# Kernel optimization log

Measured on AMD Instinct MI355X. Metric: run time of the kernel, lower is better.

The kernel has to match this reference:

```python
import jax, jax.numpy as jnp
import numpy as np

D_MODEL = 1024
N_HEADS = 16
HEAD_DIM = D_MODEL // N_HEADS
WINDOW = 128
N_PERSIST = 4
KSIZE = 3


def _make_mask(L):
    """[T,T] additive mask, T = N_PERSIST + L. Persistent rows: causal among
    persistent tokens. Sequence rows: all persistent cols + sliding causal window."""
    T = N_PERSIST + L
    r = jnp.arange(T)[:, None]
    c = jnp.arange(T)[None, :]
    seq_allowed = (c < N_PERSIST) | ((c >= jnp.maximum(N_PERSIST, r - WINDOW + 1)) & (c <= r))
    allowed = jnp.where(r < N_PERSIST, c <= r, seq_allowed)
    return jnp.where(allowed, 0.0, -jnp.inf).astype(jnp.float32)


def _causal_dw_conv(y, w, b):
    # y: [B,T,D] -> depthwise causal conv1d + SiLU -> [B,T,D]
    y = y.transpose(0, 2, 1)  # [B,D,T]
    y = jax.lax.conv_general_dilated(
        y, w, window_strides=(1,), padding=[(KSIZE - 1, 0)],
        feature_group_count=D_MODEL, dimension_numbers=('NCH', 'OIH', 'NCH'))
    y = jax.nn.silu(y + b[None, :, None])
    return y.transpose(0, 2, 1)


def _l2norm(y, eps=1e-12):
    n = jnp.linalg.norm(y, axis=-1, keepdims=True)
    return y / jnp.maximum(n, eps)


def setup_inputs() -> dict:
    key = jax.random.key(0)
    ks = jax.random.split(key, 12)
    s = 1.0 / np.sqrt(D_MODEL)
    return {
        'x': jax.random.normal(ks[0], (1, 2048, D_MODEL), jnp.float32),
        'persistent_memory': jax.random.normal(ks[1], (1, N_PERSIST, D_MODEL), jnp.float32) * 0.02,
        'Wq': jax.random.normal(ks[2], (D_MODEL, D_MODEL), jnp.float32) * s,
        'Wk': jax.random.normal(ks[3], (D_MODEL, D_MODEL), jnp.float32) * s,
        'Wv': jax.random.normal(ks[4], (D_MODEL, D_MODEL), jnp.float32) * s,
        'Wo': jax.random.normal(ks[5], (D_MODEL, D_MODEL), jnp.float32) * s,
        'q_conv_w': jax.random.normal(ks[6], (D_MODEL, 1, KSIZE), jnp.float32) * 0.3,
        'q_conv_b': jax.random.normal(ks[7], (D_MODEL,), jnp.float32) * 0.02,
        'k_conv_w': jax.random.normal(ks[8], (D_MODEL, 1, KSIZE), jnp.float32) * 0.3,
        'k_conv_b': jax.random.normal(ks[9], (D_MODEL,), jnp.float32) * 0.02,
        'v_conv_w': jax.random.normal(ks[10], (D_MODEL, 1, KSIZE), jnp.float32) * 0.3,
        'v_conv_b': jax.random.normal(ks[11], (D_MODEL,), jnp.float32) * 0.02,
    }


def reference(x, persistent_memory, Wq, Wk, Wv, Wo,
              q_conv_w, q_conv_b, k_conv_w, k_conv_b, v_conv_w, v_conv_b):
    B, L, D = x.shape
    T = L + N_PERSIST
    scale = HEAD_DIM ** -0.5
    xp = jnp.concatenate([jnp.broadcast_to(persistent_memory, (B, N_PERSIST, D)), x], axis=1)
    Q = xp @ Wq.T
    K = xp @ Wk.T
    V = xp @ Wv.T
    Q = _causal_dw_conv(Q, q_conv_w, q_conv_b)
    K = _causal_dw_conv(K, k_conv_w, k_conv_b)
    V = _causal_dw_conv(V, v_conv_w, v_conv_b)
    Q = _l2norm(Q)
    K = _l2norm(K)
    # [B,H,T,hd]
    Q = Q.reshape(B, T, N_HEADS, HEAD_DIM).transpose(0, 2, 1, 3)
    K = K.reshape(B, T, N_HEADS, HEAD_DIM).transpose(0, 2, 1, 3)
    V = V.reshape(B, T, N_HEADS, HEAD_DIM).transpose(0, 2, 1, 3)
    scores = jnp.einsum('bhqd,bhkd->bhqk', Q, K) * scale + _make_mask(L)[None, None]
    attn = jax.nn.softmax(scores, axis=-1)
    out = jnp.einsum('bhqk,bhkd->bhqd', attn, V)
    out = out.transpose(0, 2, 1, 3).reshape(B, T, D) @ Wo.T
    return out[:, N_PERSIST:, :]
```

## Files before the change

kernel.cpp:

```cpp
#include <hip/hip_runtime.h>
#include <math.h>

typedef unsigned short u16;
typedef unsigned int   u32;
typedef unsigned long long u64;
typedef __attribute__((ext_vector_type(8))) short bf16x8;
typedef __attribute__((ext_vector_type(4))) float f32x4;
typedef __attribute__((ext_vector_type(4))) int i32x4;

#define TTOT  2052
#define NPERS 4
#define LSEQ  2048
#define WIN   128
#define NHEAD 16
#define HDIM  64
#define DM    1024
#define MPAD  2176

__device__ __forceinline__ float bf2f(u16 u) {
    union { unsigned int i; float f; } v; v.i = ((unsigned int)u) << 16; return v.f;
}
__device__ __forceinline__ u16 f2bf(float f) {
    union { float f; unsigned int i; } v; v.f = f;
    unsigned int r = (v.i + 0x7fffu + ((v.i >> 16) & 1u)) >> 16;
    return (u16)r;
}
__device__ __forceinline__ u32 pk2(float lo, float hi) {
    return (u32)f2bf(lo) | ((u32)f2bf(hi) << 16);
}

__device__ __forceinline__ void glds16(const u16* g, u16* l) {
    __builtin_amdgcn_global_load_lds(
        (__attribute__((address_space(1))) void*)(g),
        (__attribute__((address_space(3))) void*)(l),
        16, 0, 0);
}

#define XP_UNITS (TTOT * DM / 4)
#define W_UNITS  (DM * DM / 4)
#define CVT_BLOCKS ((XP_UNITS + 4 * W_UNITS) / 256)

__global__ __launch_bounds__(256) void cvt(const float* __restrict__ x, const float* __restrict__ pm,
    const float* __restrict__ Wq, const float* __restrict__ Wk, const float* __restrict__ Wv,
    const float* __restrict__ Wo,
    u16* __restrict__ xp, u16* __restrict__ Wcat, u16* __restrict__ Woh)
{
    const int id = blockIdx.x * 256 + threadIdx.x;
    const float* s; u16* d;
    if (id < XP_UNITS) {
        const size_t e = (size_t)id * 4;
        const int row = (int)(e >> 10), c = (int)(e & 1023);
        s = (row < NPERS) ? (pm + (size_t)row * DM + c) : (x + (size_t)(row - NPERS) * DM + c);
        d = xp + e;
    } else {
        const int w   = id - XP_UNITS;
        const int sel = w >> 18;
        const size_t e = (size_t)(w & (W_UNITS - 1)) * 4;
        if (sel == 0)      { s = Wq + e; d = Wcat + e; }
        else if (sel == 1) { s = Wk + e; d = Wcat + (size_t)DM * DM + e; }
        else if (sel == 2) { s = Wv + e; d = Wcat + 2 * (size_t)DM * DM + e; }
        else               { s = Wo + e; d = Woh + e; }
    }
    f32x4 v = *(const f32x4*)s;
    *(u64*)d = (u64)pk2(v[0], v[1]) | ((u64)pk2(v[2], v[3]) << 32);
}

template<int TM, int TN, bool OF32>
__device__ __forceinline__ void gemm_lds(const u16* __restrict__ Ablk, const u16* __restrict__ Bblk,
                                         void* __restrict__ Cbase, int mlim)
{
    __shared__ __align__(16) u16 As[TM * 64];
    __shared__ __align__(16) u16 Bs[TN * 64];
    const int tid  = threadIdx.x;
    const int lane = tid & 63;
    const int l15  = lane & 15, quad = lane >> 4;
    constexpr int RM = TM / 32, RN = TN / 32;
    const int wm = (tid >> 7) * (TM / 2);
    const int wn = ((tid >> 6) & 1) * (TN / 2);

    f32x4 acc[RM][RN];
    #pragma unroll
    for (int i = 0; i < RM; i++)
        #pragma unroll
        for (int j = 0; j < RN; j++) acc[i][j] = (f32x4){0.f, 0.f, 0.f, 0.f};

    constexpr int LA = TM / 32;
    constexpr int LB = TN / 32;

    for (int kk = 0; kk < DM; kk += 64) {
        #pragma unroll
        for (int i = 0; i < LA; i++) {
            const int e = i * 256 + tid;
            const int row = e >> 3, sc = (e & 7) ^ (row & 7);
            glds16(Ablk + (size_t)row * DM + kk + sc * 8, As + (size_t)e * 8);
        }
        #pragma unroll
        for (int i = 0; i < LB; i++) {
            const int e = i * 256 + tid;
            const int row = e >> 3, sc = (e & 7) ^ (row & 7);
            glds16(Bblk + (size_t)row * DM + kk + sc * 8, Bs + (size_t)e * 8);
        }
        __syncthreads();
        #pragma unroll
        for (int kc = 0; kc < 2; kc++) {
            bf16x8 af[RM], bfr[RN];
            #pragma unroll
            for (int i = 0; i < RM; i++)
                af[i]  = *(const bf16x8*)&As[(wm + i * 16 + l15) * 64 + (((kc * 4 + quad) ^ (l15 & 7)) * 8)];
            #pragma unroll
            for (int j = 0; j < RN; j++)
                bfr[j] = *(const bf16x8*)&Bs[(wn + j * 16 + l15) * 64 + (((kc * 4 + quad) ^ (l15 & 7)) * 8)];
            #pragma unroll
            for (int i = 0; i < RM; i++)
                #pragma unroll
                for (int j = 0; j < RN; j++)
                    acc[i][j] = __builtin_amdgcn_mfma_f32_16x16x32_bf16(af[i], bfr[j], acc[i][j], 0, 0, 0);
        }
        __syncthreads();
    }

    #pragma unroll
    for (int i = 0; i < RM; i++) {
        const int m0 = wm + i * 16 + quad * 4;
        #pragma unroll
        for (int j = 0; j < RN; j++) {
            const int n = wn + j * 16 + l15;
            #pragma unroll
            for (int r = 0; r < 4; r++) {
                const int m = m0 + r;
                if (m < mlim) {
                    if (OF32) ((float*)Cbase)[(size_t)m * DM + n] = acc[i][j][r];
                    else      ((u16*)Cbase)[(size_t)m * DM + n]   = f2bf(acc[i][j][r]);
                }
            }
        }
    }
}

__global__ __launch_bounds__(256) void gemm_qkv(const u16* __restrict__ xp, const u16* __restrict__ Wcat,
    u16* __restrict__ Qr, u16* __restrict__ Kr, u16* __restrict__ Vr)
{
    const int Mb = blockIdx.x * 128;
    const int nb = blockIdx.y;
    u16* C = (nb < 8) ? Qr : (nb < 16) ? Kr : Vr;
    const int Ncol = (nb & 7) * 128;
    gemm_lds<128, 128, false>(xp + (size_t)Mb * DM,
                              Wcat + (size_t)nb * 128 * DM,
                              (void*)(C + (size_t)Mb * DM + Ncol),
                              TTOT - Mb);
}

__global__ __launch_bounds__(256) void gemm_out(const u16* __restrict__ AO, const u16* __restrict__ Woh,
                                                float* __restrict__ Cout)
{
    const int Mb = blockIdx.x * 64, Nb = blockIdx.y * 128;
    gemm_lds<64, 128, true>(AO + (size_t)Mb * DM, Woh + (size_t)Nb * DM,
                            (void*)(Cout + (size_t)Mb * DM + Nb), 64);
}

__global__ __launch_bounds__(256) void conv_silu_norm(
    const u16* __restrict__ Qr, const u16* __restrict__ Kr, const u16* __restrict__ Vr,
    const float* __restrict__ qw, const float* __restrict__ qb,
    const float* __restrict__ kw, const float* __restrict__ kb,
    const float* __restrict__ vw, const float* __restrict__ vb,
    u16* __restrict__ Qc, u16* __restrict__ Kc, u16* __restrict__ Vc)
{
    const int t0 = blockIdx.x * 2;
    const int z  = blockIdx.y;
    const u16* raw; const float *w, *b; u16* out;
    if (z == 0)      { raw = Qr; w = qw; b = qb; out = Qc; }
    else if (z == 1) { raw = Kr; w = kw; b = kb; out = Kc; }
    else             { raw = Vr; w = vw; b = vb; out = Vc; }

    const int tid = threadIdx.x;
    const int d0  = tid * 4;

    const u16* r0 = raw + (size_t)t0 * DM + d0;
    const u64 cm2 = (t0 >= 2) ? *(const u64*)(r0 - 2 * DM) : 0ULL;
    const u64 cm1 = (t0 >= 1) ? *(const u64*)(r0 - DM)     : 0ULL;
    const u64 c0  = *(const u64*)r0;
    const u64 c1  = *(const u64*)(r0 + DM);
    const f32x4 bias = *(const f32x4*)(b + d0);
    const f32x4 w0v  = *(const f32x4*)(w + 3 * d0);
    const f32x4 w1v  = *(const f32x4*)(w + 3 * d0 + 4);
    const f32x4 w2v  = *(const f32x4*)(w + 3 * d0 + 8);
    const float warr[12] = {w0v[0], w0v[1], w0v[2], w0v[3],
                            w1v[0], w1v[1], w1v[2], w1v[3],
                            w2v[0], w2v[1], w2v[2], w2v[3]};

    float va[4], vb2[4];
    float ss0 = 0.f, ss1 = 0.f;
    #pragma unroll
    for (int c = 0; c < 4; c++) {
        const float xm2 = bf2f((u16)(cm2 >> (16 * c)));
        const float xm1 = bf2f((u16)(cm1 >> (16 * c)));
        const float x0  = bf2f((u16)(c0  >> (16 * c)));
        const float x1  = bf2f((u16)(c1  >> (16 * c)));
        const float w0 = warr[3*c], w1 = warr[3*c + 1], w2 = warr[3*c + 2];
        float a0 = bias[c] + w2 * x0 + w1 * xm1 + w0 * xm2;
        float a1 = bias[c] + w2 * x1 + w1 * x0  + w0 * xm1;
        const float y0 = a0 / (1.f + __expf(-a0));
        const float y1 = a1 / (1.f + __expf(-a1));
        va[c] = y0; vb2[c] = y1;
        ss0 += y0 * y0; ss1 += y1 * y1;
    }
    float inv0 = 1.f, inv1 = 1.f;
    if (z < 2) {
        #pragma unroll
        for (int off = 32; off > 0; off >>= 1) {
            ss0 += __shfl_down(ss0, off, 64);
            ss1 += __shfl_down(ss1, off, 64);
        }
        __shared__ float red[8];
        const int wv = tid >> 6, ln = tid & 63;
        if (ln == 0) { red[wv] = ss0; red[wv + 4] = ss1; }
        __syncthreads();
        inv0 = 1.f / fmaxf(sqrtf(red[0] + red[1] + red[2] + red[3]), 1e-12f);
        inv1 = 1.f / fmaxf(sqrtf(red[4] + red[5] + red[6] + red[7]), 1e-12f);
    }
    u64 o0 = 0, o1 = 0;
    #pragma unroll
    for (int c = 0; c < 4; c++) {
        o0 |= (u64)f2bf(va[c]  * inv0) << (16 * c);
        o1 |= (u64)f2bf(vb2[c] * inv1) << (16 * c);
    }
    *(u64*)(out + (size_t)t0 * DM + d0)      = o0;
    *(u64*)(out + (size_t)(t0 + 1) * DM + d0) = o1;
}

#define QT     64
#define KTILES 13
#define KROWS  208
#define KPAD   224
#define KSTR   72
#define VSTR   232

__global__ __launch_bounds__(256) void attn(const u16* __restrict__ Q, const u16* __restrict__ K,
                                            const u16* __restrict__ V, u16* __restrict__ AO)
{
    const int h  = blockIdx.y;
    const int qb = blockIdx.x * QT;
    const int kstart = max(NPERS, qb + NPERS - (WIN - 1));
    const int nk = NPERS + (qb + NPERS + QT - 1) - kstart + 1;

    __shared__ __align__(16) u16 KP[KROWS * KSTR];
    __shared__ __align__(16) u16 Vt[64 * VSTR];
    u16* Ks = KP;
    u16* Ps = KP;

    const int tid = threadIdx.x;

    for (int c = tid; c < KROWS * 8; c += 256) {
        const int i = c >> 3, off = (c & 7) * 8;
        if (i < nk) {
            const int g = (i < NPERS) ? i : (kstart + i - NPERS);
            *(i32x4*)&Ks[i * KSTR + off] = *(const i32x4*)&K[(size_t)g * DM + h * HDIM + off];
        }
    }
    {
        const int d = tid & 63, w4 = tid >> 6;
        for (int i2 = w4 * 2; i2 < KPAD; i2 += 8) {
            u16 a = 0, b = 0;
            if (i2 < nk)     { const int g = (i2     < NPERS) ? i2     : (kstart + i2     - NPERS); a = V[(size_t)g * DM + h * HDIM + d]; }
            if (i2 + 1 < nk) { const int g = (i2 + 1 < NPERS) ? i2 + 1 : (kstart + i2 + 1 - NPERS); b = V[(size_t)g * DM + h * HDIM + d]; }
            *(u32*)&Vt[d * VSTR + i2] = (u32)a | ((u32)b << 16);
        }
    }
    __syncthreads();

    const int wv = tid >> 6, lane = tid & 63, l15 = lane & 15, quad = lane >> 4;
    const int qloc0 = wv * 16;

    const int tqrow = qb + qloc0 + l15 + NPERS;
    const bf16x8 qa0 = *(const bf16x8*)&Q[(size_t)tqrow * DM + h * HDIM + quad * 8];
    const bf16x8 qa1 = *(const bf16x8*)&Q[(size_t)tqrow * DM + h * HDIM + 32 + quad * 8];

    f32x4 st[KTILES];
    #pragma unroll
    for (int t = 0; t < KTILES; t++) {
        const bf16x8 kb0 = *(const bf16x8*)&Ks[(t * 16 + l15) * KSTR + quad * 8];
        const bf16x8 kb1 = *(const bf16x8*)&Ks[(t * 16 + l15) * KSTR + 32 + quad * 8];
        f32x4 z = (f32x4){0.f, 0.f, 0.f, 0.f};
        z = __builtin_amdgcn_mfma_f32_16x16x32_bf16(qa0, kb0, z, 0, 0, 0);
        z = __builtin_amdgcn_mfma_f32_16x16x32_bf16(qa1, kb1, z, 0, 0, 0);
        st[t] = z;
    }

    const float scale = 0.125f;
    float mrow[4] = {-INFINITY, -INFINITY, -INFINITY, -INFINITY};
    #pragma unroll
    for (int t = 0; t < KTILES; t++) {
        const int i  = t * 16 + l15;
        const int kg = kstart + i - NPERS;
        #pragma unroll
        for (int r = 0; r < 4; r++) {
            const int tqr = qb + qloc0 + quad * 4 + r + NPERS;
            const bool ok = (i < NPERS) || ((i < nk) && (kg >= tqr - (WIN - 1)) && (kg <= tqr));
            const float s = ok ? st[t][r] * scale : -INFINITY;
            st[t][r] = s;
            mrow[r] = fmaxf(mrow[r], s);
        }
    }
    #pragma unroll
    for (int off = 1; off < 16; off <<= 1)
        #pragma unroll
        for (int r = 0; r < 4; r++) mrow[r] = fmaxf(mrow[r], __shfl_xor(mrow[r], off, 64));

    float ssum[4] = {0.f, 0.f, 0.f, 0.f};
    #pragma unroll
    for (int t = 0; t < KTILES; t++)
        #pragma unroll
        for (int r = 0; r < 4; r++) {
            const float p = __expf(st[t][r] - mrow[r]);
            st[t][r] = p;
            ssum[r] += p;
        }
    #pragma unroll
    for (int off = 1; off < 16; off <<= 1)
        #pragma unroll
        for (int r = 0; r < 4; r++) ssum[r] += __shfl_xor(ssum[r], off, 64);
    float inv[4];
    #pragma unroll
    for (int r = 0; r < 4; r++) inv[r] = 1.f / ssum[r];

    __syncthreads();

    #pragma unroll
    for (int t = 0; t < KTILES; t++)
        #pragma unroll
        for (int r = 0; r < 4; r++)
            Ps[(qloc0 + quad * 4 + r) * VSTR + t * 16 + l15] = f2bf(st[t][r] * inv[r]);
    *(u64*)&Ps[(qloc0 + l15) * VSTR + KROWS + quad * 4] = 0ULL;
    __syncthreads();

    f32x4 oacc[4];
    #pragma unroll
    for (int dt = 0; dt < 4; dt++) oacc[dt] = (f32x4){0.f, 0.f, 0.f, 0.f};
    for (int ks = 0; ks < KPAD / 32; ks++) {
        const bf16x8 pa = *(const bf16x8*)&Ps[(qloc0 + l15) * VSTR + ks * 32 + quad * 8];
        #pragma unroll
        for (int dt = 0; dt < 4; dt++) {
            const bf16x8 vb = *(const bf16x8*)&Vt[(dt * 16 + l15) * VSTR + ks * 32 + quad * 8];
            oacc[dt] = __builtin_amdgcn_mfma_f32_16x16x32_bf16(pa, vb, oacc[dt], 0, 0, 0);
        }
    }

    #pragma unroll
    for (int dt = 0; dt < 4; dt++)
        #pragma unroll
        for (int r = 0; r < 4; r++)
            AO[(size_t)(qb + qloc0 + quad * 4 + r) * DM + h * HDIM + dt * 16 + l15] = f2bf(oacc[dt][r]);
}

extern "C" void kernel_launch(void* const* d_in, const int* in_sizes, int n_in,
                              void* d_out, int out_size, void* d_ws, size_t ws_size,
                              hipStream_t stream)
{
    const float* x  = (const float*)d_in[0];
    const float* pm = (const float*)d_in[1];
    const float* Wq = (const float*)d_in[2];
    const float* Wk = (const float*)d_in[3];
    const float* Wv = (const float*)d_in[4];
    const float* Wo = (const float*)d_in[5];
    const float* qw = (const float*)d_in[6];
    const float* qb = (const float*)d_in[7];
    const float* kw = (const float*)d_in[8];
    const float* kb = (const float*)d_in[9];
    const float* vw = (const float*)d_in[10];
    const float* vb = (const float*)d_in[11];
    float* out = (float*)d_out;

    u16* ws16 = (u16*)d_ws;
    const size_t SZ_W  = (size_t)DM * DM;
    const size_t SZ_R  = (size_t)TTOT * DM;
    const size_t SZ_XP = (size_t)MPAD * DM;
    u16* Woh  = ws16;
    u16* Qr   = Woh + SZ_W;        u16* AO = Qr;
    u16* Kr   = Qr + SZ_R;
    u16* Vr   = Kr + SZ_R;
    u16* Vc   = Vr + SZ_R;
    u16* xp   = Vc + SZ_R;         u16* Qc = xp;
    u16* Wcat = xp + SZ_XP;        u16* Kc = Wcat;

    hipLaunchKernelGGL(cvt, dim3(CVT_BLOCKS), dim3(256), 0, stream,
                       x, pm, Wq, Wk, Wv, Wo, xp, Wcat, Woh);
    hipLaunchKernelGGL(gemm_qkv, dim3(17, 24), dim3(256), 0, stream,
                       xp, Wcat, Qr, Kr, Vr);
    hipLaunchKernelGGL(conv_silu_norm, dim3(TTOT / 2, 3), dim3(256), 0, stream,
                       Qr, Kr, Vr, qw, qb, kw, kb, vw, vb, Qc, Kc, Vc);
    hipLaunchKernelGGL(attn, dim3(LSEQ / QT, NHEAD), dim3(256), 0, stream,
                       Qc, Kc, Vc, AO);
    hipLaunchKernelGGL(gemm_out, dim3(32, 8), dim3(256), 0, stream,
                       AO, Woh, out);
}
```

Before: 159.2 us.

## Prefetch V into registers, async swizzled K load, drop softmax max pass

The attention kernel now issues the V gathers into registers up front and writes them to the transposed shared-memory buffer only after the QK/softmax phase, so V load latency overlaps the score computation. K is loaded with direct global-to-LDS copies into an XOR-swizzled unpadded layout instead of padded rows. The running max and its shuffle reduction are removed because the l2-normalized Q and K keep scores bounded. The register prefetch raises VGPR pressure, and the kernel relies on a glds16 helper that must already exist in the file.

```diff
diff --git a/kernel.cpp b/kernel.cpp
--- a/kernel.cpp
+++ b/kernel.cpp
@@ -232,7 +232,6 @@
 #define KTILES 13
 #define KROWS  208
 #define KPAD   224
-#define KSTR   72
 #define VSTR   232
 
 __global__ __launch_bounds__(256) void attn(const u16* __restrict__ Q, const u16* __restrict__ K,
@@ -243,43 +242,47 @@
     const int kstart = max(NPERS, qb + NPERS - (WIN - 1));
     const int nk = NPERS + (qb + NPERS + QT - 1) - kstart + 1;
 
-    __shared__ __align__(16) u16 KP[KROWS * KSTR];
+    __shared__ __align__(16) u16 KP[64 * VSTR];
     __shared__ __align__(16) u16 Vt[64 * VSTR];
     u16* Ks = KP;
     u16* Ps = KP;
 
-    const int tid = threadIdx.x;
-
-    for (int c = tid; c < KROWS * 8; c += 256) {
-        const int i = c >> 3, off = (c & 7) * 8;
-        if (i < nk) {
-            const int g = (i < NPERS) ? i : (kstart + i - NPERS);
-            *(i32x4*)&Ks[i * KSTR + off] = *(const i32x4*)&K[(size_t)g * DM + h * HDIM + off];
-        }
-    }
-    {
-        const int d = tid & 63, w4 = tid >> 6;
-        for (int i2 = w4 * 2; i2 < KPAD; i2 += 8) {
-            u16 a = 0, b = 0;
-            if (i2 < nk)     { const int g = (i2     < NPERS) ? i2     : (kstart + i2     - NPERS); a = V[(size_t)g * DM + h * HDIM + d]; }
-            if (i2 + 1 < nk) { const int g = (i2 + 1 < NPERS) ? i2 + 1 : (kstart + i2 + 1 - NPERS); b = V[(size_t)g * DM + h * HDIM + d]; }
-            *(u32*)&Vt[d * VSTR + i2] = (u32)a | ((u32)b << 16);
+    const int tid  = threadIdx.x;
+    const int wv   = tid >> 6, lane = tid & 63, l15 = lane & 15, quad = lane >> 4;
+
+    u32 vreg[28];
+    #pragma unroll
+    for (int i = 0; i < 28; i++) {
+        const int i2 = wv * 2 + i * 8;
+        const int g0 = (i2     < NPERS) ? i2     : min(kstart + i2     - NPERS, TTOT - 1);
+        const int g1 = (i2 + 1 < NPERS) ? i2 + 1 : min(kstart + i2 + 1 - NPERS, TTOT - 1);
+        vreg[i] = (u32)V[(size_t)g0 * DM + h * HDIM + lane]
+                | ((u32)V[(size_t)g1 * DM + h * HDIM + lane] << 16);
+    }
+
+    #pragma unroll
+    for (int i = 0; i < 7; i++) {
+        const int c = i * 256 + tid;
+        if (c < KROWS * 8) {
+            const int r  = c >> 3;
+            const int sc = (c & 7) ^ (r & 7);
+            const int g  = (r < NPERS) ? r : min(kstart + r - NPERS, TTOT - 1);
+            glds16(K + (size_t)g * DM + h * HDIM + sc * 8, Ks + (size_t)c * 8);
         }
     }
     __syncthreads();
 
-    const int wv = tid >> 6, lane = tid & 63, l15 = lane & 15, quad = lane >> 4;
     const int qloc0 = wv * 16;
-
     const int tqrow = qb + qloc0 + l15 + NPERS;
     const bf16x8 qa0 = *(const bf16x8*)&Q[(size_t)tqrow * DM + h * HDIM + quad * 8];
     const bf16x8 qa1 = *(const bf16x8*)&Q[(size_t)tqrow * DM + h * HDIM + 32 + quad * 8];
 
+    const int sw = l15 & 7;
     f32x4 st[KTILES];
     #pragma unroll
     for (int t = 0; t < KTILES; t++) {
-        const bf16x8 kb0 = *(const bf16x8*)&Ks[(t * 16 + l15) * KSTR + quad * 8];
-        const bf16x8 kb1 = *(const bf16x8*)&Ks[(t * 16 + l15) * KSTR + 32 + quad * 8];
+        const bf16x8 kb0 = *(const bf16x8*)&Ks[(t * 16 + l15) * 64 + ((quad ^ sw) * 8)];
+        const bf16x8 kb1 = *(const bf16x8*)&Ks[(t * 16 + l15) * 64 + (((4 + quad) ^ sw) * 8)];
         f32x4 z = (f32x4){0.f, 0.f, 0.f, 0.f};
         z = __builtin_amdgcn_mfma_f32_16x16x32_bf16(qa0, kb0, z, 0, 0, 0);
         z = __builtin_amdgcn_mfma_f32_16x16x32_bf16(qa1, kb1, z, 0, 0, 0);
@@ -287,7 +290,7 @@
     }
 
     const float scale = 0.125f;
-    float mrow[4] = {-INFINITY, -INFINITY, -INFINITY, -INFINITY};
+    float ssum[4] = {0.f, 0.f, 0.f, 0.f};
     #pragma unroll
     for (int t = 0; t < KTILES; t++) {
         const int i  = t * 16 + l15;
@@ -296,25 +299,11 @@
         for (int r = 0; r < 4; r++) {
             const int tqr = qb + qloc0 + quad * 4 + r + NPERS;
             const bool ok = (i < NPERS) || ((i < nk) && (kg >= tqr - (WIN - 1)) && (kg <= tqr));
-            const float s = ok ? st[t][r] * scale : -INFINITY;
-            st[t][r] = s;
-            mrow[r] = fmaxf(mrow[r], s);
-        }
-    }
-    #pragma unroll
-    for (int off = 1; off < 16; off <<= 1)
-        #pragma unroll
-        for (int r = 0; r < 4; r++) mrow[r] = fmaxf(mrow[r], __shfl_xor(mrow[r], off, 64));
-
-    float ssum[4] = {0.f, 0.f, 0.f, 0.f};
-    #pragma unroll
-    for (int t = 0; t < KTILES; t++)
-        #pragma unroll
-        for (int r = 0; r < 4; r++) {
-            const float p = __expf(st[t][r] - mrow[r]);
+            const float p = ok ? __expf(st[t][r] * scale) : 0.f;
             st[t][r] = p;
             ssum[r] += p;
         }
+    }
     #pragma unroll
     for (int off = 1; off < 16; off <<= 1)
         #pragma unroll
@@ -325,6 +314,11 @@
 
     __syncthreads();
 
+    #pragma unroll
+    for (int i = 0; i < 28; i++) {
+        const int i2 = wv * 2 + i * 8;
+        *(u32*)&Vt[lane * VSTR + i2] = vreg[i];
+    }
     #pragma unroll
     for (int t = 0; t < KTILES; t++)
         #pragma unroll
```

After: 150.0 us, median of 2. -5.8%, faster.
